# Kernel tuning notes

Measured on AMD Instinct MI355X. Metric: run time of the kernel, lower is better.

## Reference

```python
import jax, jax.numpy as jnp
import numpy as np

B, N, T, F = 8, 10000, 12, 1
E, HG, HR, P = 160000, 64, 64, 12


def setup_inputs() -> dict:
    key = jax.random.key(0)
    ks = jax.random.split(key, 12)
    s = 0.05
    x = jax.random.normal(ks[0], (B, N, T, F), jnp.float32)
    edge_index = jax.random.randint(ks[1], (2, E), 0, N)
    edge_weight = jax.random.uniform(ks[2], (E,), jnp.float32)
    gcn_W = jax.random.normal(ks[3], (F, HG), jnp.float32) * s
    gcn_b = jnp.zeros((HG,), jnp.float32)
    W_ih = jax.random.normal(ks[4], (3 * HR, HG), jnp.float32) * s
    W_hh = jax.random.normal(ks[5], (3 * HR, HR), jnp.float32) * s
    b_ih = jax.random.normal(ks[6], (3 * HR,), jnp.float32) * s
    b_hh = jax.random.normal(ks[7], (3 * HR,), jnp.float32) * s
    W_out = jax.random.normal(ks[8], (P * F, HR), jnp.float32) * s
    b_out = jnp.zeros((P * F,), jnp.float32)
    return dict(x=x, edge_index=edge_index, edge_weight=edge_weight,
                gcn_W=gcn_W, gcn_b=gcn_b, W_ih=W_ih, W_hh=W_hh,
                b_ih=b_ih, b_hh=b_hh, W_out=W_out, b_out=b_out)


def reference(x, edge_index, edge_weight, gcn_W, gcn_b, W_ih, W_hh, b_ih, b_hh, W_out, b_out):
    # x: (B, N, T, F). Graph identical across batch and time, so fold
    # the per-timestep GCNConv into one batched gather/segment-sum.
    src, dst = edge_index[0], edge_index[1]
    loops = jnp.arange(N)
    # GCNConv default: add self-loops with weight 1, symmetric normalization.
    src2 = jnp.concatenate([src, loops])
    dst2 = jnp.concatenate([dst, loops])
    w2 = jnp.concatenate([edge_weight, jnp.ones((N,), edge_weight.dtype)])
    deg = jax.ops.segment_sum(w2, dst2, num_segments=N)            # (N,)
    dinv = jnp.where(deg > 0, jax.lax.rsqrt(deg), 0.0)
    norm = dinv[src2] * w2 * dinv[dst2]                            # (E+N,)
    # Aggregate raw features first (F=1, linearity lets W commute with agg).
    xn = jnp.moveaxis(x, 1, 0)                                     # (N, B, T, F)
    msg = xn[src2] * norm[:, None, None, None]                     # (E+N, B, T, F)
    agg = jax.ops.segment_sum(msg, dst2, num_segments=N)           # (N, B, T, F)
    h = jax.nn.relu(agg @ gcn_W + gcn_b)                           # (N, B, T, HG)
    # -> (T, B*N, HG) matching torch's reshape(B*N, T, HG)
    seq = h.transpose(2, 1, 0, 3).reshape(T, B * N, HG)

    def gru_step(hprev, xt):
        gi = xt @ W_ih.T + b_ih
        gh = hprev @ W_hh.T + b_hh
        ir, iz, inn = jnp.split(gi, 3, axis=-1)
        hr, hz, hn = jnp.split(gh, 3, axis=-1)
        r = jax.nn.sigmoid(ir + hr)
        z = jax.nn.sigmoid(iz + hz)
        n = jnp.tanh(inn + r * hn)
        hnew = (1.0 - z) * n + z * hprev
        return hnew, None

    h0 = jnp.zeros((B * N, HR), x.dtype)
    hlast, _ = jax.lax.scan(gru_step, h0, seq)                     # (B*N, HR)
    # dropout is identity in eval mode
    pred = hlast @ W_out.T + b_out                                 # (B*N, P*F)
    return pred.reshape(B, N, P)  # F == 1 -> squeeze(-1)
```

## Files before the change

kernel.cpp:

```cpp
#include <hip/hip_runtime.h>

#define N_NODES 10000
#define B 8
#define T_STEPS 12
#define E_EDGES 160000
#define HG 64
#define HR 64
#define P_OUT 12
#define BN (B * N_NODES)
#define CAP 48

typedef __attribute__((ext_vector_type(8))) short short8;
typedef __attribute__((ext_vector_type(4))) float f32x4;

__device__ __forceinline__ short f2bf(float f) {
    unsigned u = __builtin_bit_cast(unsigned, f);
    u += 0x7FFFu + ((u >> 16) & 1u);
    return (short)(u >> 16);
}


__global__ void fillprep_kernel(const int* __restrict__ ei, const float* __restrict__ ew,
                                float* __restrict__ deg, int* __restrict__ cursor,
                                int2* __restrict__ csr,
                                const float* __restrict__ Wih, const float* __restrict__ Whh,
                                const float* __restrict__ Wout,
                                short* __restrict__ Wihb, short* __restrict__ Whhb,
                                short* __restrict__ Woutb) {
    if (blockIdx.x < 625) {
        int e = blockIdx.x * 256 + threadIdx.x;
        int s = ei[e];
        int d = ei[E_EDGES + e];
        float w = ew[e];
        atomicAdd(&deg[d], w);
        int pos = atomicAdd(&cursor[d], 1);
        if (pos < CAP)
            csr[d * CAP + pos] = make_int2(s, __float_as_int(w));
    } else {
        int i = (blockIdx.x - 625) * 256 + threadIdx.x;
        if (i < 192 * 64) {
            Wihb[i] = f2bf(Wih[i]);
            Whhb[i] = f2bf(Whh[i]);
        }
        if (i < 16 * 64) {
            int p = i >> 6, k = i & 63;
            Woutb[i] = (p < P_OUT) ? f2bf(Wout[p * 64 + k]) : (short)0;
        }
    }
}


__device__ __forceinline__ float fast_rcp(float v) { return __builtin_amdgcn_rcpf(v); }
__device__ __forceinline__ float sigmoid_f(float v) { return fast_rcp(1.0f + __expf(-v)); }
__device__ __forceinline__ float tanh_f(float v) {
    float e = __expf(-2.0f * v);
    return fmaf(2.0f, fast_rcp(1.0f + e), -1.0f);
}

__global__ __launch_bounds__(256, 2) void gru_mfma_kernel(
    const float* __restrict__ x, const float* __restrict__ deg,
    const int* __restrict__ cnt, const int2* __restrict__ csr,
    const float* __restrict__ gW, const float* __restrict__ gb,
    const short* __restrict__ Wihb, const short* __restrict__ Whhb,
    const float* __restrict__ bih, const float* __restrict__ bhh,
    const short* __restrict__ Woutb, const float* __restrict__ bout,
    float* __restrict__ out)
{
    __shared__ short hlds[64 * 64];
    __shared__ short xlds[64 * 64];
    __shared__ float a_sh[12][64];
    const int tid = threadIdx.x;
    const int w   = tid >> 6;
    const int wu  = __builtin_amdgcn_readfirstlane(w);
    const int l   = tid & 63;
    const int lr  = l & 15;
    const int qu  = l >> 4;
    const int blk = blockIdx.x;

    {
        const int sub = l & 3;
        const int seq = wu * 16 + (l >> 2);
        const int bn  = blk * 64 + seq;
        const int n   = bn % N_NODES;
        const int b   = bn / N_NODES;
        const float di = rsqrtf(deg[n] + 1.0f);
        float4 A0 = {0.f,0.f,0.f,0.f}, A1 = {0.f,0.f,0.f,0.f}, A2 = {0.f,0.f,0.f,0.f};
        const int c = min(cnt[n], CAP);
        const int2* cp = &csr[n * CAP];
#pragma unroll 2
        for (int i = sub; i < c; i += 4) {
            int2 pr = cp[i];
            float we = __int_as_float(pr.y) * rsqrtf(deg[pr.x] + 1.0f);
            const float4* xs = (const float4*)&x[(b * N_NODES + pr.x) * T_STEPS];
            float4 x0 = xs[0], x1 = xs[1], x2 = xs[2];
            A0.x = fmaf(we, x0.x, A0.x); A0.y = fmaf(we, x0.y, A0.y);
            A0.z = fmaf(we, x0.z, A0.z); A0.w = fmaf(we, x0.w, A0.w);
            A1.x = fmaf(we, x1.x, A1.x); A1.y = fmaf(we, x1.y, A1.y);
            A1.z = fmaf(we, x1.z, A1.z); A1.w = fmaf(we, x1.w, A1.w);
            A2.x = fmaf(we, x2.x, A2.x); A2.y = fmaf(we, x2.y, A2.y);
            A2.z = fmaf(we, x2.z, A2.z); A2.w = fmaf(we, x2.w, A2.w);
        }
#pragma unroll
        for (int m = 1; m <= 2; m <<= 1) {
            A0.x += __shfl_xor(A0.x, m); A0.y += __shfl_xor(A0.y, m);
            A0.z += __shfl_xor(A0.z, m); A0.w += __shfl_xor(A0.w, m);
            A1.x += __shfl_xor(A1.x, m); A1.y += __shfl_xor(A1.y, m);
            A1.z += __shfl_xor(A1.z, m); A1.w += __shfl_xor(A1.w, m);
            A2.x += __shfl_xor(A2.x, m); A2.y += __shfl_xor(A2.y, m);
            A2.z += __shfl_xor(A2.z, m); A2.w += __shfl_xor(A2.w, m);
        }
        if (sub == 0) {
            const float4* xn = (const float4*)&x[(b * N_NODES + n) * T_STEPS];
            float4 x0 = xn[0], x1 = xn[1], x2 = xn[2];
            a_sh[0][seq]  = di * fmaf(di, x0.x, A0.x);
            a_sh[1][seq]  = di * fmaf(di, x0.y, A0.y);
            a_sh[2][seq]  = di * fmaf(di, x0.z, A0.z);
            a_sh[3][seq]  = di * fmaf(di, x0.w, A0.w);
            a_sh[4][seq]  = di * fmaf(di, x1.x, A1.x);
            a_sh[5][seq]  = di * fmaf(di, x1.y, A1.y);
            a_sh[6][seq]  = di * fmaf(di, x1.z, A1.z);
            a_sh[7][seq]  = di * fmaf(di, x1.w, A1.w);
            a_sh[8][seq]  = di * fmaf(di, x2.x, A2.x);
            a_sh[9][seq]  = di * fmaf(di, x2.y, A2.y);
            a_sh[10][seq] = di * fmaf(di, x2.z, A2.z);
            a_sh[11][seq] = di * fmaf(di, x2.w, A2.w);
        }
    }

    short8 bIr[2], bIz[2], bIn[2], bHr[2], bHz[2], bHn[2];
#pragma unroll
    for (int kt = 0; kt < 2; kt++) {
        const int ko = kt * 32 + qu * 8;
        bIr[kt] = *(const short8*)&Wihb[(      16 * wu + lr) * 64 + ko];
        bIz[kt] = *(const short8*)&Wihb[( 64 + 16 * wu + lr) * 64 + ko];
        bIn[kt] = *(const short8*)&Wihb[(128 + 16 * wu + lr) * 64 + ko];
        bHr[kt] = *(const short8*)&Whhb[(      16 * wu + lr) * 64 + ko];
        bHz[kt] = *(const short8*)&Whhb[( 64 + 16 * wu + lr) * 64 + ko];
        bHn[kt] = *(const short8*)&Whhb[(128 + 16 * wu + lr) * 64 + ko];
    }
    float gwv[16], gbv[16];
#pragma unroll
    for (int j = 0; j < 16; j++) { gwv[j] = gW[wu * 16 + j]; gbv[j] = gb[wu * 16 + j]; }

    const int u = 16 * w + lr;
    const float bR  = bih[u]       + bhh[u];
    const float bZ  = bih[u + 64]  + bhh[u + 64];
    const float bIN = bih[u + 128];
    const float bHN = bhh[u + 128];
    const int uc = u >> 3;
    const int u7 = u & 7;

    float h_c[4][4];
#pragma unroll
    for (int mt = 0; mt < 4; mt++)
#pragma unroll
        for (int r = 0; r < 4; r++) h_c[mt][r] = 0.0f;
    {
        short8 z = (short8){0,0,0,0,0,0,0,0};
        *(short8*)&hlds[l * 64 + ((2 * w) << 3)]     = z;
        *(short8*)&hlds[l * 64 + ((2 * w + 1) << 3)] = z;
    }
    __syncthreads();

#pragma unroll 1
    for (int t = 0; t < T_STEPS; t++) {
        {
            const float a = a_sh[t][l];
            short8 c0, c1;
#pragma unroll
            for (int j = 0; j < 8; j++) {
                c0[j] = f2bf(fmaxf(fmaf(a, gwv[j],     gbv[j]),     0.0f));
                c1[j] = f2bf(fmaxf(fmaf(a, gwv[8 + j], gbv[8 + j]), 0.0f));
            }
            const int s3 = l & 7;
            *(short8*)&xlds[l * 64 + (((2 * w)     ^ s3) << 3)] = c0;
            *(short8*)&xlds[l * 64 + (((2 * w + 1) ^ s3) << 3)] = c1;
        }
        __syncthreads();

        f32x4 accR[4], accZ[4], accNX[4], accNH[4];
#pragma unroll
        for (int mt = 0; mt < 4; mt++) {
            accR[mt]  = (f32x4){bR,  bR,  bR,  bR};
            accZ[mt]  = (f32x4){bZ,  bZ,  bZ,  bZ};
            accNX[mt] = (f32x4){bIN, bIN, bIN, bIN};
            accNH[mt] = (f32x4){bHN, bHN, bHN, bHN};
        }

#pragma unroll
        for (int mt = 0; mt < 4; mt++) {
            const int seq = mt * 16 + lr;
            const int s3 = seq & 7;
            short8 ax0 = *(const short8*)&xlds[seq * 64 + (((0 + qu) ^ s3) << 3)];
            short8 ax1 = *(const short8*)&xlds[seq * 64 + (((4 + qu) ^ s3) << 3)];
            short8 ah0 = *(const short8*)&hlds[seq * 64 + (((0 + qu) ^ s3) << 3)];
            short8 ah1 = *(const short8*)&hlds[seq * 64 + (((4 + qu) ^ s3) << 3)];

            accR[mt]  = __builtin_amdgcn_mfma_f32_16x16x32_bf16(ax0, bIr[0], accR[mt], 0, 0, 0);
            accR[mt]  = __builtin_amdgcn_mfma_f32_16x16x32_bf16(ax1, bIr[1], accR[mt], 0, 0, 0);
            accR[mt]  = __builtin_amdgcn_mfma_f32_16x16x32_bf16(ah0, bHr[0], accR[mt], 0, 0, 0);
            accR[mt]  = __builtin_amdgcn_mfma_f32_16x16x32_bf16(ah1, bHr[1], accR[mt], 0, 0, 0);
            accZ[mt]  = __builtin_amdgcn_mfma_f32_16x16x32_bf16(ax0, bIz[0], accZ[mt], 0, 0, 0);
            accZ[mt]  = __builtin_amdgcn_mfma_f32_16x16x32_bf16(ax1, bIz[1], accZ[mt], 0, 0, 0);
            accZ[mt]  = __builtin_amdgcn_mfma_f32_16x16x32_bf16(ah0, bHz[0], accZ[mt], 0, 0, 0);
            accZ[mt]  = __builtin_amdgcn_mfma_f32_16x16x32_bf16(ah1, bHz[1], accZ[mt], 0, 0, 0);
            accNX[mt] = __builtin_amdgcn_mfma_f32_16x16x32_bf16(ax0, bIn[0], accNX[mt], 0, 0, 0);
            accNX[mt] = __builtin_amdgcn_mfma_f32_16x16x32_bf16(ax1, bIn[1], accNX[mt], 0, 0, 0);
            accNH[mt] = __builtin_amdgcn_mfma_f32_16x16x32_bf16(ah0, bHn[0], accNH[mt], 0, 0, 0);
            accNH[mt] = __builtin_amdgcn_mfma_f32_16x16x32_bf16(ah1, bHn[1], accNH[mt], 0, 0, 0);
        }
        __syncthreads();

#pragma unroll
        for (int mt = 0; mt < 4; mt++) {
#pragma unroll
            for (int r = 0; r < 4; r++) {
                const int seq = mt * 16 + qu * 4 + r;
                float pr = sigmoid_f(accR[mt][r]);
                float pz = sigmoid_f(accZ[mt][r]);
                float pn = tanh_f(fmaf(pr, accNH[mt][r], accNX[mt][r]));
                float hn = fmaf(pz, h_c[mt][r] - pn, pn);
                h_c[mt][r] = hn;
                hlds[seq * 64 + ((uc ^ (seq & 7)) << 3) + u7] = f2bf(hn);
            }
        }
    }
    __syncthreads();

    short8 bWo[2];
#pragma unroll
    for (int kt = 0; kt < 2; kt++)
        bWo[kt] = *(const short8*)&Woutb[lr * 64 + kt * 32 + qu * 8];
    const float bo = (lr < P_OUT) ? bout[lr] : 0.0f;

    f32x4 accO = (f32x4){0.f, 0.f, 0.f, 0.f};
    {
        const int seq = w * 16 + lr;
        const int s3 = seq & 7;
        short8 ah0 = *(const short8*)&hlds[seq * 64 + (((0 + qu) ^ s3) << 3)];
        short8 ah1 = *(const short8*)&hlds[seq * 64 + (((4 + qu) ^ s3) << 3)];
        accO = __builtin_amdgcn_mfma_f32_16x16x32_bf16(ah0, bWo[0], accO, 0, 0, 0);
        accO = __builtin_amdgcn_mfma_f32_16x16x32_bf16(ah1, bWo[1], accO, 0, 0, 0);
    }
    if (lr < P_OUT) {
#pragma unroll
        for (int r = 0; r < 4; r++) {
            const int seq = w * 16 + qu * 4 + r;
            out[(blk * 64 + seq) * P_OUT + lr] = accO[r] + bo;
        }
    }
}


extern "C" void kernel_launch(void* const* d_in, const int* in_sizes, int n_in,
                              void* d_out, int out_size, void* d_ws, size_t ws_size,
                              hipStream_t stream)
{
    const float* x    = (const float*)d_in[0];
    const int*   ei   = (const int*)  d_in[1];
    const float* ew   = (const float*)d_in[2];
    const float* gW   = (const float*)d_in[3];
    const float* gb   = (const float*)d_in[4];
    const float* Wih  = (const float*)d_in[5];
    const float* Whh  = (const float*)d_in[6];
    const float* bih  = (const float*)d_in[7];
    const float* bhh  = (const float*)d_in[8];
    const float* Wout = (const float*)d_in[9];
    const float* bout = (const float*)d_in[10];
    float* out = (float*)d_out;

    float* deg    = (float*)d_ws;
    int*   cursor = (int*)(deg + N_NODES);
    int2*  csr    = (int2*)(cursor + N_NODES);
    short* Wihb   = (short*)(csr + N_NODES * CAP);
    short* Whhb   = Wihb + 192 * 64;
    short* Woutb  = Whhb + 192 * 64;

    hipMemsetAsync(deg, 0, 2 * N_NODES * sizeof(float), stream);
    fillprep_kernel<<<673, 256, 0, stream>>>(ei, ew, deg, cursor, csr,
                                             Wih, Whh, Wout, Wihb, Whhb, Woutb);
    gru_mfma_kernel<<<BN / 64, 256, 0, stream>>>(x, deg, cursor, csr, gW, gb,
                                                 Wihb, Whhb, bih, bhh,
                                                 Woutb, bout, out);
}
```

Measured before the change: 178.6 us.

## Partition CSR build by destination range with LDS atomics, drop memset

The edge-binning kernel now gives each of 40 blocks a contiguous range of 250 destination nodes. Every block scans all edges and uses shared-memory atomics for degree and slot counters, then writes deg and count to global memory. This removes the global atomics and the separate hipMemsetAsync launch. In exchange, each block reads the full 160000-entry dst array, and only 40 blocks do the fill, so parallelism is low and total read traffic is much higher.

```diff
diff --git a/kernel.cpp b/kernel.cpp
--- a/kernel.cpp
+++ b/kernel.cpp
@@ -9,6 +9,8 @@
 #define P_OUT 12
 #define BN (B * N_NODES)
 #define CAP 48
+#define FILL_NB 40
+#define NPB 250
 
 typedef __attribute__((ext_vector_type(8))) short short8;
 typedef __attribute__((ext_vector_type(4))) float f32x4;
@@ -19,25 +21,39 @@
     return (short)(u >> 16);
 }
 
-
-__global__ void fillprep_kernel(const int* __restrict__ ei, const float* __restrict__ ew,
-                                float* __restrict__ deg, int* __restrict__ cursor,
-                                int2* __restrict__ csr,
-                                const float* __restrict__ Wih, const float* __restrict__ Whh,
-                                const float* __restrict__ Wout,
-                                short* __restrict__ Wihb, short* __restrict__ Whhb,
-                                short* __restrict__ Woutb) {
-    if (blockIdx.x < 625) {
-        int e = blockIdx.x * 256 + threadIdx.x;
-        int s = ei[e];
-        int d = ei[E_EDGES + e];
-        float w = ew[e];
-        atomicAdd(&deg[d], w);
-        int pos = atomicAdd(&cursor[d], 1);
-        if (pos < CAP)
-            csr[d * CAP + pos] = make_int2(s, __float_as_int(w));
+__global__ __launch_bounds__(256) void fill_kernel(
+    const int* __restrict__ ei, const float* __restrict__ ew,
+    float* __restrict__ deg, int* __restrict__ cnt, int2* __restrict__ csr,
+    const float* __restrict__ Wih, const float* __restrict__ Whh,
+    const float* __restrict__ Wout,
+    short* __restrict__ Wihb, short* __restrict__ Whhb, short* __restrict__ Woutb)
+{
+    if (blockIdx.x < FILL_NB) {
+        __shared__ float sdeg[NPB];
+        __shared__ int   scnt[NPB];
+        const int n0 = blockIdx.x * NPB;
+        for (int i = threadIdx.x; i < NPB; i += 256) { sdeg[i] = 0.0f; scnt[i] = 0; }
+        __syncthreads();
+#pragma unroll 4
+        for (int e = threadIdx.x; e < E_EDGES; e += 256) {
+            int d  = ei[E_EDGES + e];
+            unsigned dl = (unsigned)(d - n0);
+            if (dl < NPB) {
+                float wv = ew[e];
+                int s = ei[e];
+                atomicAdd(&sdeg[dl], wv);
+                int pos = atomicAdd(&scnt[dl], 1);
+                if (pos < CAP)
+                    csr[d * CAP + pos] = make_int2(s, __float_as_int(wv));
+            }
+        }
+        __syncthreads();
+        for (int i = threadIdx.x; i < NPB; i += 256) {
+            deg[n0 + i] = sdeg[i];
+            cnt[n0 + i] = scnt[i];
+        }
     } else {
-        int i = (blockIdx.x - 625) * 256 + threadIdx.x;
+        int i = (blockIdx.x - FILL_NB) * 256 + threadIdx.x;
         if (i < 192 * 64) {
             Wihb[i] = f2bf(Wih[i]);
             Whhb[i] = f2bf(Whh[i]);
@@ -269,17 +285,16 @@
     const float* bout = (const float*)d_in[10];
     float* out = (float*)d_out;
 
-    float* deg    = (float*)d_ws;
-    int*   cursor = (int*)(deg + N_NODES);
-    int2*  csr    = (int2*)(cursor + N_NODES);
-    short* Wihb   = (short*)(csr + N_NODES * CAP);
-    short* Whhb   = Wihb + 192 * 64;
-    short* Woutb  = Whhb + 192 * 64;
-
-    hipMemsetAsync(deg, 0, 2 * N_NODES * sizeof(float), stream);
-    fillprep_kernel<<<673, 256, 0, stream>>>(ei, ew, deg, cursor, csr,
-                                             Wih, Whh, Wout, Wihb, Whhb, Woutb);
-    gru_mfma_kernel<<<BN / 64, 256, 0, stream>>>(x, deg, cursor, csr, gW, gb,
+    float* deg   = (float*)d_ws;
+    int*   cnt   = (int*)(deg + N_NODES);
+    int2*  csr   = (int2*)(cnt + N_NODES);
+    short* Wihb  = (short*)(csr + N_NODES * CAP);
+    short* Whhb  = Wihb + 192 * 64;
+    short* Woutb = Whhb + 192 * 64;
+
+    fill_kernel<<<FILL_NB + 48, 256, 0, stream>>>(ei, ew, deg, cnt, csr,
+                                                  Wih, Whh, Wout, Wihb, Whhb, Woutb);
+    gru_mfma_kernel<<<BN / 64, 256, 0, stream>>>(x, deg, cnt, csr, gW, gb,
                                                  Wihb, Whhb, bih, bhh,
                                                  Woutb, bout, out);
 }
```

Result: slower. 522.4 us (+192.4%).
